# Kernel optimization log

Hardware: AMD Instinct MI355X
Metric: run time of the kernel (lower is better)

The kernel has to match this reference:

```python
import jax, jax.numpy as jnp
import numpy as np

# Instant-NGP / tcnn hash grid encoding constants (from init_kwargs)
L = 16           # n_levels
F = 2            # n_features_per_level
T = 2 ** 15      # hashmap size per level
DIM = 3
BASE = 16.0      # base_resolution
FINEST = 512.0   # finest_resolution
RANGE = 1.0
B = (FINEST / BASE) ** (1.0 / (L - 1))  # per_level_scale
N_POINTS = 500000
# tcnn spatial hash primes (first dim uses 1)
PRIMES = jnp.array([1, 2654435761, 805459861], dtype=jnp.uint32)


def setup_inputs() -> dict:
    key = jax.random.key(0)
    k1, k2 = jax.random.split(key)
    x = jax.random.uniform(k1, (N_POINTS, DIM), dtype=jnp.float32)  # points in [0,1)
    table = jax.random.normal(k2, (L, T, F), dtype=jnp.float32) * 1e-4  # tcnn-style tiny init
    return {"x": x, "table": table}


def reference(x, table):
    # wrapper: map from [-range, range] to [0, 1]
    xn = (x + RANGE) / (2.0 * RANGE)                       # [N, 3]
    n = xn.shape[0]
    # per-level grid scale (tcnn: scale = base * b^l - 1)
    scales = BASE * (B ** jnp.arange(L, dtype=jnp.float32)) - 1.0  # [L]
    pos = xn[:, None, :] * scales[None, :, None] + 0.5     # [N, L, 3]
    pos_floor = jnp.floor(pos)
    frac = pos - pos_floor                                  # [N, L, 3]
    grid = pos_floor.astype(jnp.uint32)                    # [N, L, 3]
    # 8 cube corners as binary offsets
    corners = jnp.array([[(c >> d) & 1 for d in range(DIM)] for c in range(2 ** DIM)],
                        dtype=jnp.uint32)                   # [8, 3]
    coords = grid[:, :, None, :] + corners[None, None, :, :]  # [N, L, 8, 3] uint32
    h = coords * PRIMES                                     # uint32 wraps (modular mult)
    idx = (h[..., 0] ^ h[..., 1] ^ h[..., 2]) & jnp.uint32(T - 1)  # [N, L, 8]
    # gather per-level features: [N, L, 8, F]
    feats = table[jnp.arange(L)[None, :, None], idx]
    # trilinear interpolation weights
    cf = corners.astype(jnp.float32)                        # [8, 3]
    w = jnp.prod(jnp.where(cf[None, None, :, :] == 1.0,
                           frac[:, :, None, :],
                           1.0 - frac[:, :, None, :]), axis=-1)  # [N, L, 8]
    out = jnp.einsum('nlc,nlcf->nlf', w, feats)             # [N, L, F]
    return out.reshape(n, L * F)
```

## Files before the change

kernel.cpp:

```cpp
#include <hip/hip_runtime.h>
#include <hip/hip_fp16.h>
#include <stdint.h>


constexpr int      kL  = 16;
constexpr int      kT  = 32768;
constexpr uint32_t kM  = kT - 1;
constexpr uint32_t kP1 = 2654435761u;
constexpr uint32_t kP2 = 805459861u;
constexpr int      kNC = 16;
constexpr int      kBT = 1024;

typedef float f32x2 __attribute__((ext_vector_type(2)));

__device__ __constant__ float c_scales[kL] = {
    15.0f,
    19.158736798317972f,
    24.398416831491190f,
    31.0f,
    39.317473596635944f,
    49.796833662982380f,
    63.0f,
    79.634947193271890f,
    100.59366732596477f,
    127.0f,
    160.26989438654378f,
    202.18733465192953f,
    255.0f,
    321.53978877308750f,
    405.37466930385903f,
    511.0f
};

__device__ __forceinline__ void load3(float (&v)[3], const float* __restrict__ x, int n) {
    v[0] = x[n * 3 + 0];
    v[1] = x[n * 3 + 1];
    v[2] = x[n * 3 + 2];
}

__device__ __forceinline__ void issue8(
    const uint32_t* __restrict__ ltab, float s, const float (&xv)[3],
    uint32_t (&buf)[8], float (&w)[8])
{
    float p0 = fmaf((xv[0] + 1.0f) * 0.5f, s, 0.5f);
    float p1 = fmaf((xv[1] + 1.0f) * 0.5f, s, 0.5f);
    float p2 = fmaf((xv[2] + 1.0f) * 0.5f, s, 0.5f);

    float fl0 = floorf(p0), fl1 = floorf(p1), fl2 = floorf(p2);
    float fr0 = p0 - fl0,   fr1 = p1 - fl1,   fr2 = p2 - fl2;

    uint32_t g0 = (uint32_t)(int)fl0;
    uint32_t g1 = (uint32_t)(int)fl1;
    uint32_t g2 = (uint32_t)(int)fl2;

    uint32_t hx0 = g0;        uint32_t hx1 = g0 + 1u;
    uint32_t hy0 = g1 * kP1;  uint32_t hy1 = hy0 + kP1;
    uint32_t hz0 = g2 * kP2;  uint32_t hz1 = hz0 + kP2;

    float wy0 = 1.0f - fr1, wz0 = 1.0f - fr2;
    float wx0 = 1.0f - fr0;

    uint32_t hyz[4];
    float    wyz[4];
    hyz[0] = hy0 ^ hz0;  wyz[0] = wy0 * wz0;
    hyz[1] = hy1 ^ hz0;  wyz[1] = fr1 * wz0;
    hyz[2] = hy0 ^ hz1;  wyz[2] = wy0 * fr2;
    hyz[3] = hy1 ^ hz1;  wyz[3] = fr1 * fr2;

#pragma unroll
    for (int cc = 0; cc < 8; ++cc) {
        uint32_t hx = (cc & 1) ? hx1 : hx0;
        uint32_t idx = (hx ^ hyz[cc >> 1]) & kM;
        w[cc]   = ((cc & 1) ? fr0 : wx0) * wyz[cc >> 1];
        buf[cc] = ltab[idx];
    }
}

__device__ __forceinline__ f32x2 consume8(const uint32_t (&buf)[8], const float (&w)[8]) {
    __half2 acc = __float2half2_rn(0.0f);
#pragma unroll
    for (int cc = 0; cc < 8; ++cc) {
        __half2 h = *reinterpret_cast<const __half2*>(&buf[cc]);
        acc = __hfma2(__float2half2_rn(w[cc]), h, acc);
    }
    f32x2 r;
    r.x = __low2float(acc);
    r.y = __high2float(acc);
    return r;
}

__global__ __launch_bounds__(kBT, 4) void hashgrid_fwd(
    const float*  __restrict__ x,
    const float2* __restrict__ table,
    f32x2*        __restrict__ out,
    int n_points, int chunk_sz)
{
    __shared__ uint32_t ltab[kT];

    int bid = blockIdx.x;
    int l   = bid >> 4;
    int c   = bid & 15;

    const float4* tsrc4 = reinterpret_cast<const float4*>(table + (size_t)l * kT);
    for (int e = threadIdx.x; e < kT / 2; e += kBT) {
        float4 q = tsrc4[e];
        uint2 pp;
        pp.x = ((uint32_t)__half_as_ushort(__float2half_rn(q.y)) << 16)
             |  (uint32_t)__half_as_ushort(__float2half_rn(q.x));
        pp.y = ((uint32_t)__half_as_ushort(__float2half_rn(q.w)) << 16)
             |  (uint32_t)__half_as_ushort(__float2half_rn(q.z));
        *reinterpret_cast<uint2*>(&ltab[e * 2]) = pp;
    }
    __syncthreads();

    float s    = c_scales[l];
    int   base = c * chunk_sz;
    int   lim  = min(base + chunk_sz, n_points);
    int   nmax = lim - 1;
    int   iters = (chunk_sz + kBT - 1) / kBT;

    uint32_t bufA[8], bufB[8];
    float    wA[8],  wB[8];
    float    xA[3],  xB[3];

    int nA = base + (int)threadIdx.x;
    load3(xA, x, min(nA, nmax));
    load3(xB, x, min(nA + kBT, nmax));

    issue8(ltab, s, xA, bufA, wA);
    __builtin_amdgcn_sched_barrier(0);

    for (int it = 0; it < iters; it += 2) {
        if (it + 1 < iters) issue8(ltab, s, xB, bufB, wB);
        load3(xA, x, min(nA + 2 * kBT, nmax));
        __builtin_amdgcn_sched_barrier(0);
        {
            f32x2 r = consume8(bufA, wA);
            if (nA < lim) out[(size_t)nA * kL + l] = r;
        }
        if (it + 2 < iters) issue8(ltab, s, xA, bufA, wA);
        load3(xB, x, min(nA + 3 * kBT, nmax));
        __builtin_amdgcn_sched_barrier(0);
        if (it + 1 < iters) {
            f32x2 r = consume8(bufB, wB);
            int nB = nA + kBT;
            if (nB < lim) out[(size_t)nB * kL + l] = r;
        }
        nA += 2 * kBT;
    }
}

extern "C" void kernel_launch(void* const* d_in, const int* in_sizes, int n_in,
                              void* d_out, int out_size, void* d_ws, size_t ws_size,
                              hipStream_t stream) {
    const float*  x     = (const float*)d_in[0];
    const float2* table = (const float2*)d_in[1];
    f32x2*        out   = (f32x2*)d_out;

    int n_points = in_sizes[0] / 3;
    int chunk_sz = (n_points + kNC - 1) / kNC;
    int blocks   = kL * kNC;

    hashgrid_fwd<<<blocks, kBT, 0, stream>>>(x, table, out, n_points, chunk_sz);
}
```

Baseline: 49.78 us.

## Restructure hash-grid pipeline with unguarded main loop and deferred weight computation

Issues the shared-memory gathers for two points back to back and defers trilinear weight computation to consume time, carrying only the three fractional coordinates between stages. This is meant to cut live registers (no eight weights per buffer). The main loop runs a guard-free even number of iterations with no min() clamps, and a separate tail loop handles the remaining points. The trade-off is less overlap between gather latency and arithmetic, since both gathers now wait behind one barrier, plus extra code for the tail.

Measured after the change: 49.78 us. No clear change (-0.0%).

```diff
diff --git a/kernel.cpp b/kernel.cpp
--- a/kernel.cpp
+++ b/kernel.cpp
@@ -38,50 +38,60 @@
     v[2] = x[n * 3 + 2];
 }
 
-__device__ __forceinline__ void issue8(
+__device__ __forceinline__ void hash_issue(
     const uint32_t* __restrict__ ltab, float s, const float (&xv)[3],
-    uint32_t (&buf)[8], float (&w)[8])
+    float (&fr)[3], uint32_t (&buf)[8])
 {
     float p0 = fmaf((xv[0] + 1.0f) * 0.5f, s, 0.5f);
     float p1 = fmaf((xv[1] + 1.0f) * 0.5f, s, 0.5f);
     float p2 = fmaf((xv[2] + 1.0f) * 0.5f, s, 0.5f);
 
     float fl0 = floorf(p0), fl1 = floorf(p1), fl2 = floorf(p2);
-    float fr0 = p0 - fl0,   fr1 = p1 - fl1,   fr2 = p2 - fl2;
+    fr[0] = p0 - fl0;  fr[1] = p1 - fl1;  fr[2] = p2 - fl2;
 
     uint32_t g0 = (uint32_t)(int)fl0;
     uint32_t g1 = (uint32_t)(int)fl1;
     uint32_t g2 = (uint32_t)(int)fl2;
 
-    uint32_t hx0 = g0;        uint32_t hx1 = g0 + 1u;
+    uint32_t g0p = g0 + 1u;
     uint32_t hy0 = g1 * kP1;  uint32_t hy1 = hy0 + kP1;
     uint32_t hz0 = g2 * kP2;  uint32_t hz1 = hz0 + kP2;
 
-    float wy0 = 1.0f - fr1, wz0 = 1.0f - fr2;
-    float wx0 = 1.0f - fr0;
+    uint32_t hyz0 = hy0 ^ hz0;
+    uint32_t hyz1 = hy1 ^ hz0;
+    uint32_t hyz2 = hy0 ^ hz1;
+    uint32_t hyz3 = hy1 ^ hz1;
 
-    uint32_t hyz[4];
-    float    wyz[4];
-    hyz[0] = hy0 ^ hz0;  wyz[0] = wy0 * wz0;
-    hyz[1] = hy1 ^ hz0;  wyz[1] = fr1 * wz0;
-    hyz[2] = hy0 ^ hz1;  wyz[2] = wy0 * fr2;
-    hyz[3] = hy1 ^ hz1;  wyz[3] = fr1 * fr2;
-
-#pragma unroll
-    for (int cc = 0; cc < 8; ++cc) {
-        uint32_t hx = (cc & 1) ? hx1 : hx0;
-        uint32_t idx = (hx ^ hyz[cc >> 1]) & kM;
-        w[cc]   = ((cc & 1) ? fr0 : wx0) * wyz[cc >> 1];
-        buf[cc] = ltab[idx];
-    }
+    buf[0] = ltab[(g0  ^ hyz0) & kM];
+    buf[1] = ltab[(g0p ^ hyz0) & kM];
+    buf[2] = ltab[(g0  ^ hyz1) & kM];
+    buf[3] = ltab[(g0p ^ hyz1) & kM];
+    buf[4] = ltab[(g0  ^ hyz2) & kM];
+    buf[5] = ltab[(g0p ^ hyz2) & kM];
+    buf[6] = ltab[(g0  ^ hyz3) & kM];
+    buf[7] = ltab[(g0p ^ hyz3) & kM];
 }
 
-__device__ __forceinline__ f32x2 consume8(const uint32_t (&buf)[8], const float (&w)[8]) {
+__device__ __forceinline__ f32x2 wconsume(const float (&fr)[3], const uint32_t (&buf)[8]) {
+    float wx0 = 1.0f - fr[0];
+    float wy0 = 1.0f - fr[1];
+    float wz0 = 1.0f - fr[2];
+    float wyz0 = wy0  * wz0;
+    float wyz1 = fr[1] * wz0;
+    float wyz2 = wy0  * fr[2];
+    float wyz3 = fr[1] * fr[2];
+
+    float wf[8];
+    wf[0] = wx0   * wyz0;  wf[1] = fr[0] * wyz0;
+    wf[2] = wx0   * wyz1;  wf[3] = fr[0] * wyz1;
+    wf[4] = wx0   * wyz2;  wf[5] = fr[0] * wyz2;
+    wf[6] = wx0   * wyz3;  wf[7] = fr[0] * wyz3;
+
     __half2 acc = __float2half2_rn(0.0f);
 #pragma unroll
     for (int cc = 0; cc < 8; ++cc) {
         __half2 h = *reinterpret_cast<const __half2*>(&buf[cc]);
-        acc = __hfma2(__float2half2_rn(w[cc]), h, acc);
+        acc = __hfma2(__float2half2_rn(wf[cc]), h, acc);
     }
     f32x2 r;
     r.x = __low2float(acc);
@@ -114,39 +124,49 @@
     __syncthreads();
 
     float s    = c_scales[l];
+    int   tid  = (int)threadIdx.x;
     int   base = c * chunk_sz;
     int   lim  = min(base + chunk_sz, n_points);
-    int   nmax = lim - 1;
-    int   iters = (chunk_sz + kBT - 1) / kBT;
 
-    uint32_t bufA[8], bufB[8];
-    float    wA[8],  wB[8];
-    float    xA[3],  xB[3];
+    int unguarded = (chunk_sz / kBT) & ~1;
 
-    int nA = base + (int)threadIdx.x;
-    load3(xA, x, min(nA, nmax));
-    load3(xB, x, min(nA + kBT, nmax));
+    int n = base + tid;
+    float xc0[3], xc1[3];
+    load3(xc0, x, n);
+    load3(xc1, x, n + kBT);
 
-    issue8(ltab, s, xA, bufA, wA);
-    __builtin_amdgcn_sched_barrier(0);
+    for (int it = 0; it < unguarded; it += 2) {
+        float    fr0[3], fr1[3];
+        uint32_t b0[8],  b1[8];
 
-    for (int it = 0; it < iters; it += 2) {
-        if (it + 1 < iters) issue8(ltab, s, xB, bufB, wB);
-        load3(xA, x, min(nA + 2 * kBT, nmax));
+        hash_issue(ltab, s, xc0, fr0, b0);
+        hash_issue(ltab, s, xc1, fr1, b1);
         __builtin_amdgcn_sched_barrier(0);
-        {
-            f32x2 r = consume8(bufA, wA);
-            if (nA < lim) out[(size_t)nA * kL + l] = r;
-        }
-        if (it + 2 < iters) issue8(ltab, s, xA, bufA, wA);
-        load3(xB, x, min(nA + 3 * kBT, nmax));
-        __builtin_amdgcn_sched_barrier(0);
-        if (it + 1 < iters) {
-            f32x2 r = consume8(bufB, wB);
-            int nB = nA + kBT;
-            if (nB < lim) out[(size_t)nB * kL + l] = r;
-        }
-        nA += 2 * kBT;
+
+        bool last = (it + 2 >= unguarded);
+        int  np0  = last ? n : n + 2 * kBT;
+        int  np1  = last ? n : n + 3 * kBT;
+        float xn0[3], xn1[3];
+        load3(xn0, x, np0);
+        load3(xn1, x, np1);
+
+        f32x2 r0 = wconsume(fr0, b0);
+        out[(size_t)n * kL + l] = r0;
+        f32x2 r1 = wconsume(fr1, b1);
+        out[(size_t)(n + kBT) * kL + l] = r1;
+
+#pragma unroll
+        for (int k = 0; k < 3; ++k) { xc0[k] = xn0[k]; xc1[k] = xn1[k]; }
+        n += 2 * kBT;
+    }
+
+    for (int nG = base + tid + unguarded * kBT; nG < lim; nG += kBT) {
+        float xv[3];
+        load3(xv, x, nG);
+        float fr[3]; uint32_t b[8];
+        hash_issue(ltab, s, xv, fr, b);
+        f32x2 r = wconsume(fr, b);
+        out[(size_t)nG * kL + l] = r;
     }
 }
 
```
